# Kernel optimization log

Measured on AMD Instinct MI355X. Metric: run time of the kernel, lower is better.

Reference implementation:

```python
import jax, jax.numpy as jnp
import numpy as np

N_TYPES = 4
AEV_DIM = 384
HIDDEN = [160, 128, 96]
CELU_ALPHA = 0.1


def _init_params(key):
    dims = [AEV_DIM] + HIDDEN + [1]
    params = {}
    for li in range(len(dims) - 1):
        key, kw = jax.random.split(key)
        scale = 1.0 / np.sqrt(dims[li])
        # stacked over the N_TYPES per-atom-type experts
        params[f"W{li}"] = (jax.random.normal(kw, (N_TYPES, dims[li], dims[li + 1]), dtype=jnp.float32) * scale)
        params[f"b{li}"] = jnp.zeros((N_TYPES, dims[li + 1]), dtype=jnp.float32)
    return params


def setup_inputs() -> dict:
    key = jax.random.key(0)
    k1, k2, k3 = jax.random.split(key, 3)
    B, A = 2048, 64
    species = jax.random.randint(k1, (B, A), 0, N_TYPES, dtype=jnp.int64)
    aev = jax.random.normal(k2, (B, A, AEV_DIM), dtype=jnp.float32)
    inp = {"species": species, "aev": aev}
    inp.update(_init_params(k3))
    return inp


def _mlp(x, t, W0, b0, W1, b1, W2, b2, W3, b3):
    # x: [N, aev_dim] -> [N] per-atom energy for atom type t
    h = jax.nn.celu(x @ W0[t] + b0[t], alpha=CELU_ALPHA)
    h = jax.nn.celu(h @ W1[t] + b1[t], alpha=CELU_ALPHA)
    h = jax.nn.celu(h @ W2[t] + b2[t], alpha=CELU_ALPHA)
    return (h @ W3[t] + b3[t]).reshape(-1)


def reference(species, aev, W0, b0, W1, b1, W2, b2, W3, b3):
    B, A = species.shape
    sp = species.reshape(-1)            # [B*A]
    x = aev.reshape(-1, aev.shape[-1])  # [B*A, aev_dim]
    out = jnp.zeros(sp.shape, dtype=aev.dtype)  # padding_fill = 0
    for t in range(N_TYPES):  # fixed small expert set
        y = _mlp(x, t, W0, b0, W1, b1, W2, b2, W3, b3)
        out = jnp.where(sp == t, y, out)
    energies = out.reshape(B, A).sum(axis=1)  # reduce over atoms
    return species, energies
```

## Files before the change

### kernel.cpp

```cpp
#include <hip/hip_runtime.h>
#include <hip/hip_bf16.h>
#include <math.h>


#define NATOMS   131072
#define NMOL     2048
#define AEV      384
#define NTYPES   4
#define MBLK     64
#define PADTOT   (NATOMS + NTYPES * MBLK)
#define NBLK_MLP (PADTOT / MBLK)
#define NBLK_H   512

#define WB_L1 61440
#define WB_L2 81920
#define WB_T  94208

typedef __attribute__((ext_vector_type(8))) short bf16x8;
typedef __attribute__((ext_vector_type(4))) float f32x4;

__device__ __forceinline__ float celu01(float v) {
  return (v > 0.f) ? v : 0.1f * (__expf(v * 10.f) - 1.f);
}
__device__ __forceinline__ unsigned short f2bf(float x) {
  unsigned u = __float_as_uint(x);
  return (unsigned short)((u + 0x7FFFu + ((u >> 16) & 1u)) >> 16);
}
__device__ __forceinline__ unsigned int pk2(float lo, float hi) {
  union { __hip_bfloat162 h; unsigned int u; } c;
  c.h = __float22bfloat162_rn(make_float2(lo, hi));
  return c.u;
}
__device__ __forceinline__ bf16x8 cvt8(const float4 r0, const float4 r1) {
  union { unsigned int u[4]; bf16x8 v; } c;
  c.u[0] = pk2(r0.x, r0.y);
  c.u[1] = pk2(r0.z, r0.w);
  c.u[2] = pk2(r1.x, r1.y);
  c.u[3] = pk2(r1.z, r1.w);
  return c.v;
}
__device__ __forceinline__ void dma16(const unsigned short* g, unsigned short* l) {
  __builtin_amdgcn_global_load_lds(
      (const __attribute__((address_space(1))) void*)(g),
      (__attribute__((address_space(3))) void*)(l), 16, 0, 0);
}


__global__ void k_pre(const int* __restrict__ species, float* __restrict__ out,
                      int* __restrict__ perm, int* __restrict__ hist,
                      const float* __restrict__ W0, const float* __restrict__ W1,
                      const float* __restrict__ W2, unsigned short* __restrict__ WB) {
  const int tid = threadIdx.x, blk = blockIdx.x;
  const int i = blk * 256 + tid;
  perm[i] = -1;
  if (i < NATOMS) out[i] = (float)species[i];
  if (i < NMOL) out[NATOMS + i] = 0.f;

  for (int f = i; f < NTYPES * WB_T; f += PADTOT) {
    const int t = f / WB_T, e0 = f - t * WB_T;
    int base, NT, N;
    const float* W;
    if (e0 < WB_L1)      { base = 0;     NT = 10; N = 160; W = W0 + (size_t)t * AEV * 160; }
    else if (e0 < WB_L2) { base = WB_L1; NT = 8;  N = 128; W = W1 + (size_t)t * 160 * 128; }
    else                 { base = WB_L2; NT = 6;  N = 96;  W = W2 + (size_t)t * 128 * 96; }
    const int e = e0 - base, frag = e >> 9, r = e & 511, lane = r >> 3, j = r & 7;
    const int kt = frag / NT, nt = frag - kt * NT;
    const int k = kt * 32 + ((lane >> 4) << 3) + j, n = nt * 16 + (lane & 15);
    WB[(size_t)t * WB_T + e0] = f2bf(W[k * N + n]);
  }

  if (blk < NBLK_H) {
    const int sp = species[i];
    const int wv = tid >> 6;
    __shared__ int wc[4 * NTYPES];
#pragma unroll
    for (int t = 0; t < NTYPES; ++t) {
      const unsigned long long m = __ballot(sp == t);
      if ((tid & 63) == 0) wc[wv * NTYPES + t] = __popcll(m);
    }
    __syncthreads();
    if (tid < NTYPES)
      hist[tid * NBLK_H + blk] = wc[tid] + wc[4 + tid] + wc[8 + tid] + wc[12 + tid];
  }
}


__global__ void k_scan(const int* __restrict__ hist, int* __restrict__ poff,
                       int* __restrict__ boff) {
  __shared__ int tot[NTYPES], base[NTYPES];
  const int tid = threadIdx.x, wv = tid >> 6, lane = tid & 63;
  int s = 0;
  for (int c = 0; c < 8; ++c) s += hist[wv * NBLK_H + c * 64 + lane];
  for (int off = 32; off; off >>= 1) s += __shfl_down(s, off);
  if (lane == 0) tot[wv] = s;
  __syncthreads();
  if (tid == 0) {
    int acc = 0; poff[0] = 0;
    for (int t = 0; t < NTYPES; ++t) {
      base[t] = acc;
      acc += ((tot[t] + 63) >> 6) << 6;
      poff[t + 1] = acc;
    }
  }
  __syncthreads();
  int carry = base[wv];
  for (int c = 0; c < 8; ++c) {
    const int orig = hist[wv * NBLK_H + c * 64 + lane];
    int v = orig;
    for (int off = 1; off < 64; off <<= 1) {
      const int u = __shfl_up(v, off);
      if (lane >= off) v += u;
    }
    boff[wv * NBLK_H + c * 64 + lane] = carry + v - orig;
    carry += __shfl(v, 63);
  }
}

__global__ void k_scatter(const int* __restrict__ species, const int* __restrict__ boff,
                          int* __restrict__ perm) {
  const int tid = threadIdx.x, blk = blockIdx.x;
  const int i = blk * 256 + tid;
  const int sp = species[i];
  const int wv = tid >> 6;
  __shared__ int wc[4 * NTYPES];
  unsigned long long msel = 0;
#pragma unroll
  for (int t = 0; t < NTYPES; ++t) {
    const unsigned long long m = __ballot(sp == t);
    if ((tid & 63) == 0) wc[wv * NTYPES + t] = __popcll(m);
    if (sp == t) msel = m;
  }
  __syncthreads();
  int woff = 0;
  for (int w = 0; w < wv; ++w) woff += wc[w * NTYPES + sp];
  const int rk = __builtin_amdgcn_mbcnt_hi((unsigned)(msel >> 32),
                 __builtin_amdgcn_mbcnt_lo((unsigned)msel, 0));
  perm[boff[sp * NBLK_H + blk] + woff + rk] = i;
}


__global__ __launch_bounds__(128) void k_mlp(
    const float* __restrict__ aev, const unsigned short* __restrict__ WB,
    const float* __restrict__ b0, const float* __restrict__ b1,
    const float* __restrict__ b2, const float* __restrict__ b3,
    const float* __restrict__ W3,
    const int* __restrict__ poff, const int* __restrict__ perm,
    float* __restrict__ outE)
{
  __shared__ __align__(16) unsigned short H[64 * 168];
  __shared__ __align__(16) unsigned short WL[2][5120];
  __shared__ int permS[64];

  const int tid  = threadIdx.x;
  const int lane = tid & 63;
  const int wv   = __builtin_amdgcn_readfirstlane(tid >> 6);
  const int quad = lane >> 4, l15 = lane & 15;
  const int slot0 = blockIdx.x * MBLK;

  if (tid < 64) permS[tid] = perm[slot0 + tid];
  int t_ = (slot0 >= poff[1]) + (slot0 >= poff[2]) + (slot0 >= poff[3]);
  if (t_ > 3) t_ = 3;
  const int t = __builtin_amdgcn_readfirstlane(t_);

  const unsigned short* WBt = WB + (size_t)t * WB_T;

#pragma unroll
  for (int s = 0; s < 5; ++s)
    dma16(WBt + (wv * 5 + s) * 512 + lane * 8, &WL[0][(wv * 5 + s) * 512]);

  __syncthreads();

  const float* rp[2];
#pragma unroll
  for (int mtl = 0; mtl < 2; ++mtl) {
    const int ai = permS[(2 * wv + mtl) * 16 + l15];
    rp[mtl] = aev + (size_t)(ai < 0 ? 0 : ai) * AEV + quad * 8;
  }

  f32x4 acc0[10][2];
#pragma unroll
  for (int nt = 0; nt < 10; ++nt) {
    const float b = b0[t * 160 + nt * 16 + l15];
#pragma unroll
    for (int mtl = 0; mtl < 2; ++mtl) acc0[nt][mtl] = (f32x4){b, b, b, b};
  }

  float4 raw[2][2];
#pragma unroll
  for (int mtl = 0; mtl < 2; ++mtl) {
    raw[mtl][0] = *(const float4*)(rp[mtl]);
    raw[mtl][1] = *(const float4*)(rp[mtl] + 4);
  }

  for (int ks = 0; ks < 12; ++ks) {
    const int cur = ks & 1;
    const bf16x8 a0 = cvt8(raw[0][0], raw[0][1]);
    const bf16x8 a1 = cvt8(raw[1][0], raw[1][1]);
    if (ks < 11) {
#pragma unroll
      for (int mtl = 0; mtl < 2; ++mtl) {
        const float* p = rp[mtl] + (ks + 1) * 32;
        raw[mtl][0] = *(const float4*)p;
        raw[mtl][1] = *(const float4*)(p + 4);
      }
#pragma unroll
      for (int s = 0; s < 5; ++s)
        dma16(WBt + ((ks + 1) * 10 + wv * 5 + s) * 512 + lane * 8,
              &WL[cur ^ 1][(wv * 5 + s) * 512]);
    } else {
#pragma unroll
      for (int s = 0; s < 4; ++s)
        dma16(WBt + WB_L1 + (wv * 4 + s) * 512 + lane * 8,
              &WL[cur ^ 1][(wv * 4 + s) * 512]);
    }
#pragma unroll
    for (int nt = 0; nt < 10; ++nt) {
      const bf16x8 w = *(const bf16x8*)&WL[cur][nt * 512 + lane * 8];
      acc0[nt][0] = __builtin_amdgcn_mfma_f32_16x16x32_bf16(a0, w, acc0[nt][0], 0, 0, 0);
      acc0[nt][1] = __builtin_amdgcn_mfma_f32_16x16x32_bf16(a1, w, acc0[nt][1], 0, 0, 0);
    }
    __syncthreads();
  }

#pragma unroll
  for (int nt = 0; nt < 10; ++nt)
#pragma unroll
    for (int mtl = 0; mtl < 2; ++mtl)
#pragma unroll
      for (int r = 0; r < 4; ++r)
        H[((2 * wv + mtl) * 16 + quad * 4 + r) * 168 + nt * 16 + l15] = f2bf(celu01(acc0[nt][mtl][r]));
  __syncthreads();

  f32x4 acc1[8][2];
#pragma unroll
  for (int nt = 0; nt < 8; ++nt) {
    const float b = b1[t * 128 + nt * 16 + l15];
#pragma unroll
    for (int mtl = 0; mtl < 2; ++mtl) acc1[nt][mtl] = (f32x4){b, b, b, b};
  }
  for (int ks = 0; ks < 5; ++ks) {
    const int cur = ks & 1;
    const bf16x8 a0 = *(const bf16x8*)&H[((2 * wv + 0) * 16 + l15) * 168 + quad * 8 + ks * 32];
    const bf16x8 a1 = *(const bf16x8*)&H[((2 * wv + 1) * 16 + l15) * 168 + quad * 8 + ks * 32];
    if (ks < 4) {
#pragma unroll
      for (int s = 0; s < 4; ++s)
        dma16(WBt + WB_L1 + ((ks + 1) * 8 + wv * 4 + s) * 512 + lane * 8,
              &WL[cur ^ 1][(wv * 4 + s) * 512]);
    } else {
#pragma unroll
      for (int s = 0; s < 3; ++s)
        dma16(WBt + WB_L2 + (wv * 3 + s) * 512 + lane * 8,
              &WL[cur ^ 1][(wv * 3 + s) * 512]);
    }
#pragma unroll
    for (int nt = 0; nt < 8; ++nt) {
      const bf16x8 w = *(const bf16x8*)&WL[cur][nt * 512 + lane * 8];
      acc1[nt][0] = __builtin_amdgcn_mfma_f32_16x16x32_bf16(a0, w, acc1[nt][0], 0, 0, 0);
      acc1[nt][1] = __builtin_amdgcn_mfma_f32_16x16x32_bf16(a1, w, acc1[nt][1], 0, 0, 0);
    }
    __syncthreads();
  }
#pragma unroll
  for (int nt = 0; nt < 8; ++nt)
#pragma unroll
    for (int mtl = 0; mtl < 2; ++mtl)
#pragma unroll
      for (int r = 0; r < 4; ++r)
        H[((2 * wv + mtl) * 16 + quad * 4 + r) * 136 + nt * 16 + l15] = f2bf(celu01(acc1[nt][mtl][r]));
  __syncthreads();

  f32x4 acc2[6][2];
#pragma unroll
  for (int nt = 0; nt < 6; ++nt) {
    const float b = b2[t * 96 + nt * 16 + l15];
#pragma unroll
    for (int mtl = 0; mtl < 2; ++mtl) acc2[nt][mtl] = (f32x4){b, b, b, b};
  }
  for (int ks = 0; ks < 4; ++ks) {
    const int cur = (ks + 1) & 1;
    const bf16x8 a0 = *(const bf16x8*)&H[((2 * wv + 0) * 16 + l15) * 136 + quad * 8 + ks * 32];
    const bf16x8 a1 = *(const bf16x8*)&H[((2 * wv + 1) * 16 + l15) * 136 + quad * 8 + ks * 32];
    if (ks < 3) {
#pragma unroll
      for (int s = 0; s < 3; ++s)
        dma16(WBt + WB_L2 + ((ks + 1) * 6 + wv * 3 + s) * 512 + lane * 8,
              &WL[cur ^ 1][(wv * 3 + s) * 512]);
    }
#pragma unroll
    for (int nt = 0; nt < 6; ++nt) {
      const bf16x8 w = *(const bf16x8*)&WL[cur][nt * 512 + lane * 8];
      acc2[nt][0] = __builtin_amdgcn_mfma_f32_16x16x32_bf16(a0, w, acc2[nt][0], 0, 0, 0);
      acc2[nt][1] = __builtin_amdgcn_mfma_f32_16x16x32_bf16(a1, w, acc2[nt][1], 0, 0, 0);
    }
    __syncthreads();
  }
#pragma unroll
  for (int nt = 0; nt < 6; ++nt)
#pragma unroll
    for (int mtl = 0; mtl < 2; ++mtl)
#pragma unroll
      for (int r = 0; r < 4; ++r)
        H[((2 * wv + mtl) * 16 + quad * 4 + r) * 104 + nt * 16 + l15] = f2bf(celu01(acc2[nt][mtl][r]));
  __syncthreads();

  bf16x8 w3f[3];
#pragma unroll
  for (int ks = 0; ks < 3; ++ks) {
    const float* wp = W3 + t * 96 + ks * 32 + quad * 8;
    const float4 f0 = *(const float4*)wp;
    const float4 f1 = *(const float4*)(wp + 4);
    w3f[ks] = cvt8(f0, f1);
  }
  f32x4 accE[2];
#pragma unroll
  for (int mtl = 0; mtl < 2; ++mtl) accE[mtl] = (f32x4){0.f, 0.f, 0.f, 0.f};
#pragma unroll
  for (int mtl = 0; mtl < 2; ++mtl)
#pragma unroll
    for (int ks = 0; ks < 3; ++ks) {
      const bf16x8 a = *(const bf16x8*)&H[((2 * wv + mtl) * 16 + l15) * 104 + quad * 8 + ks * 32];
      accE[mtl] = __builtin_amdgcn_mfma_f32_16x16x32_bf16(a, w3f[ks], accE[mtl], 0, 0, 0);
    }
  const float bb3 = b3[t];
#pragma unroll
  for (int mtl = 0; mtl < 2; ++mtl)
#pragma unroll
    for (int r = 0; r < 4; ++r)
      if (l15 == 0) {
        const int ai = permS[(2 * wv + mtl) * 16 + quad * 4 + r];
        if (ai >= 0) atomicAdd(&outE[ai >> 6], accE[mtl][r] + bb3);
      }
}


extern "C" void kernel_launch(void* const* d_in, const int* in_sizes, int n_in,
                              void* d_out, int out_size, void* d_ws, size_t ws_size,
                              hipStream_t stream)
{
  const int*   species = (const int*)d_in[0];
  const float* aev     = (const float*)d_in[1];
  const float* W0 = (const float*)d_in[2];
  const float* b0 = (const float*)d_in[3];
  const float* W1 = (const float*)d_in[4];
  const float* b1 = (const float*)d_in[5];
  const float* W2 = (const float*)d_in[6];
  const float* b2 = (const float*)d_in[7];
  const float* W3 = (const float*)d_in[8];
  const float* b3 = (const float*)d_in[9];
  float* out = (float*)d_out;

  int* poff = (int*)d_ws;
  int* hist = poff + 8;
  int* boff = hist + NTYPES * NBLK_H;
  int* perm = boff + NTYPES * NBLK_H;
  unsigned short* WB = (unsigned short*)(perm + PADTOT);

  k_pre    <<<PADTOT / 256, 256, 0, stream>>>(species, out, perm, hist, W0, W1, W2, WB);
  k_scan   <<<1, 256, 0, stream>>>(hist, poff, boff);
  k_scatter<<<NBLK_H, 256, 0, stream>>>(species, boff, perm);
  k_mlp    <<<NBLK_MLP, 128, 0, stream>>>(aev, WB, b0, b1, b2, b3, W3,
                                          poff, perm, out + NATOMS);
}
```

Measured before the change: 367.3 us.

## Use single-wave MLP blocks loading weights directly from global memory

Shrinks each MLP block to one wavefront handling 32 atoms and drops the LDS double-buffered weight staging along with all block barriers. Weight fragments are now read straight from global memory, expected to hit in L2/L1, and the permutation indices move from LDS to wave shuffles. The goal is to remove synchronization overhead and LDS traffic and to raise occupancy through more, smaller blocks. In exchange, every wave re-fetches the full weight set per 32 rows, so global and cache traffic for weights roughly doubles, and MFMA issue may stall on load latency.

```diff
diff --git a/kernel.cpp b/kernel.cpp
--- a/kernel.cpp
+++ b/kernel.cpp
@@ -8,8 +8,9 @@
 #define AEV      384
 #define NTYPES   4
 #define MBLK     64
+#define MROWS    32
 #define PADTOT   (NATOMS + NTYPES * MBLK)
-#define NBLK_MLP (PADTOT / MBLK)
+#define NBLK_MLP (PADTOT / MROWS)
 #define NBLK_H   512
 
 #define WB_L1 61440
@@ -38,11 +39,6 @@
   c.u[2] = pk2(r1.x, r1.y);
   c.u[3] = pk2(r1.z, r1.w);
   return c.v;
-}
-__device__ __forceinline__ void dma16(const unsigned short* g, unsigned short* l) {
-  __builtin_amdgcn_global_load_lds(
-      (const __attribute__((address_space(1))) void*)(g),
-      (__attribute__((address_space(3))) void*)(l), 16, 0, 0);
 }
 
 
@@ -139,7 +135,7 @@
 }
 
 
-__global__ __launch_bounds__(128) void k_mlp(
+__global__ __launch_bounds__(64) void k_mlp(
     const float* __restrict__ aev, const unsigned short* __restrict__ WB,
     const float* __restrict__ b0, const float* __restrict__ b1,
     const float* __restrict__ b2, const float* __restrict__ b3,
@@ -147,35 +143,27 @@
     const int* __restrict__ poff, const int* __restrict__ perm,
     float* __restrict__ outE)
 {
-  __shared__ __align__(16) unsigned short H[64 * 168];
-  __shared__ __align__(16) unsigned short WL[2][5120];
-  __shared__ int permS[64];
-
-  const int tid  = threadIdx.x;
-  const int lane = tid & 63;
-  const int wv   = __builtin_amdgcn_readfirstlane(tid >> 6);
+  __shared__ __align__(16) unsigned short H[MROWS * 168];
+
+  const int lane = threadIdx.x;
   const int quad = lane >> 4, l15 = lane & 15;
-  const int slot0 = blockIdx.x * MBLK;
-
-  if (tid < 64) permS[tid] = perm[slot0 + tid];
+  const int slot0 = blockIdx.x * MROWS;
+
+  const int permv = perm[slot0 + (lane & 31)];
   int t_ = (slot0 >= poff[1]) + (slot0 >= poff[2]) + (slot0 >= poff[3]);
   if (t_ > 3) t_ = 3;
   const int t = __builtin_amdgcn_readfirstlane(t_);
 
-  const unsigned short* WBt = WB + (size_t)t * WB_T;
-
-#pragma unroll
-  for (int s = 0; s < 5; ++s)
-    dma16(WBt + (wv * 5 + s) * 512 + lane * 8, &WL[0][(wv * 5 + s) * 512]);
-
-  __syncthreads();
-
   const float* rp[2];
 #pragma unroll
   for (int mtl = 0; mtl < 2; ++mtl) {
-    const int ai = permS[(2 * wv + mtl) * 16 + l15];
+    const int ai = __shfl(permv, mtl * 16 + l15);
     rp[mtl] = aev + (size_t)(ai < 0 ? 0 : ai) * AEV + quad * 8;
   }
+
+  const bf16x8* wb0 = (const bf16x8*)(WB + (size_t)t * WB_T);
+  const bf16x8* wb1 = (const bf16x8*)(WB + (size_t)t * WB_T + WB_L1);
+  const bf16x8* wb2 = (const bf16x8*)(WB + (size_t)t * WB_T + WB_L2);
 
   f32x4 acc0[10][2];
 #pragma unroll
@@ -193,7 +181,6 @@
   }
 
   for (int ks = 0; ks < 12; ++ks) {
-    const int cur = ks & 1;
     const bf16x8 a0 = cvt8(raw[0][0], raw[0][1]);
     const bf16x8 a1 = cvt8(raw[1][0], raw[1][1]);
     if (ks < 11) {
@@ -203,33 +190,22 @@
         raw[mtl][0] = *(const float4*)p;
         raw[mtl][1] = *(const float4*)(p + 4);
       }
-#pragma unroll
-      for (int s = 0; s < 5; ++s)
-        dma16(WBt + ((ks + 1) * 10 + wv * 5 + s) * 512 + lane * 8,
-              &WL[cur ^ 1][(wv * 5 + s) * 512]);
-    } else {
-#pragma unroll
-      for (int s = 0; s < 4; ++s)
-        dma16(WBt + WB_L1 + (wv * 4 + s) * 512 + lane * 8,
-              &WL[cur ^ 1][(wv * 4 + s) * 512]);
     }
 #pragma unroll
     for (int nt = 0; nt < 10; ++nt) {
-      const bf16x8 w = *(const bf16x8*)&WL[cur][nt * 512 + lane * 8];
+      const bf16x8 w = wb0[(ks * 10 + nt) * 64 + lane];
       acc0[nt][0] = __builtin_amdgcn_mfma_f32_16x16x32_bf16(a0, w, acc0[nt][0], 0, 0, 0);
       acc0[nt][1] = __builtin_amdgcn_mfma_f32_16x16x32_bf16(a1, w, acc0[nt][1], 0, 0, 0);
     }
-    __syncthreads();
-  }
-
+  }
 #pragma unroll
   for (int nt = 0; nt < 10; ++nt)
 #pragma unroll
     for (int mtl = 0; mtl < 2; ++mtl)
 #pragma unroll
       for (int r = 0; r < 4; ++r)
-        H[((2 * wv + mtl) * 16 + quad * 4 + r) * 168 + nt * 16 + l15] = f2bf(celu01(acc0[nt][mtl][r]));
-  __syncthreads();
+        H[(mtl * 16 + quad * 4 + r) * 168 + nt * 16 + l15] = f2bf(celu01(acc0[nt][mtl][r]));
+  __builtin_amdgcn_sched_barrier(0);
 
   f32x4 acc1[8][2];
 #pragma unroll
@@ -238,37 +214,26 @@
 #pragma unroll
     for (int mtl = 0; mtl < 2; ++mtl) acc1[nt][mtl] = (f32x4){b, b, b, b};
   }
+#pragma unroll
   for (int ks = 0; ks < 5; ++ks) {
-    const int cur = ks & 1;
-    const bf16x8 a0 = *(const bf16x8*)&H[((2 * wv + 0) * 16 + l15) * 168 + quad * 8 + ks * 32];
-    const bf16x8 a1 = *(const bf16x8*)&H[((2 * wv + 1) * 16 + l15) * 168 + quad * 8 + ks * 32];
-    if (ks < 4) {
-#pragma unroll
-      for (int s = 0; s < 4; ++s)
-        dma16(WBt + WB_L1 + ((ks + 1) * 8 + wv * 4 + s) * 512 + lane * 8,
-              &WL[cur ^ 1][(wv * 4 + s) * 512]);
-    } else {
-#pragma unroll
-      for (int s = 0; s < 3; ++s)
-        dma16(WBt + WB_L2 + (wv * 3 + s) * 512 + lane * 8,
-              &WL[cur ^ 1][(wv * 3 + s) * 512]);
-    }
+    const bf16x8 a0 = *(const bf16x8*)&H[(0 * 16 + l15) * 168 + quad * 8 + ks * 32];
+    const bf16x8 a1 = *(const bf16x8*)&H[(1 * 16 + l15) * 168 + quad * 8 + ks * 32];
 #pragma unroll
     for (int nt = 0; nt < 8; ++nt) {
-      const bf16x8 w = *(const bf16x8*)&WL[cur][nt * 512 + lane * 8];
+      const bf16x8 w = wb1[(ks * 8 + nt) * 64 + lane];
       acc1[nt][0] = __builtin_amdgcn_mfma_f32_16x16x32_bf16(a0, w, acc1[nt][0], 0, 0, 0);
       acc1[nt][1] = __builtin_amdgcn_mfma_f32_16x16x32_bf16(a1, w, acc1[nt][1], 0, 0, 0);
     }
-    __syncthreads();
-  }
+  }
+  __builtin_amdgcn_sched_barrier(0);
 #pragma unroll
   for (int nt = 0; nt < 8; ++nt)
 #pragma unroll
     for (int mtl = 0; mtl < 2; ++mtl)
 #pragma unroll
       for (int r = 0; r < 4; ++r)
-        H[((2 * wv + mtl) * 16 + quad * 4 + r) * 136 + nt * 16 + l15] = f2bf(celu01(acc1[nt][mtl][r]));
-  __syncthreads();
+        H[(mtl * 16 + quad * 4 + r) * 136 + nt * 16 + l15] = f2bf(celu01(acc1[nt][mtl][r]));
+  __builtin_amdgcn_sched_barrier(0);
 
   f32x4 acc2[6][2];
 #pragma unroll
@@ -277,32 +242,26 @@
 #pragma unroll
     for (int mtl = 0; mtl < 2; ++mtl) acc2[nt][mtl] = (f32x4){b, b, b, b};
   }
+#pragma unroll
   for (int ks = 0; ks < 4; ++ks) {
-    const int cur = (ks + 1) & 1;
-    const bf16x8 a0 = *(const bf16x8*)&H[((2 * wv + 0) * 16 + l15) * 136 + quad * 8 + ks * 32];
-    const bf16x8 a1 = *(const bf16x8*)&H[((2 * wv + 1) * 16 + l15) * 136 + quad * 8 + ks * 32];
-    if (ks < 3) {
-#pragma unroll
-      for (int s = 0; s < 3; ++s)
-        dma16(WBt + WB_L2 + ((ks + 1) * 6 + wv * 3 + s) * 512 + lane * 8,
-              &WL[cur ^ 1][(wv * 3 + s) * 512]);
-    }
+    const bf16x8 a0 = *(const bf16x8*)&H[(0 * 16 + l15) * 136 + quad * 8 + ks * 32];
+    const bf16x8 a1 = *(const bf16x8*)&H[(1 * 16 + l15) * 136 + quad * 8 + ks * 32];
 #pragma unroll
     for (int nt = 0; nt < 6; ++nt) {
-      const bf16x8 w = *(const bf16x8*)&WL[cur][nt * 512 + lane * 8];
+      const bf16x8 w = wb2[(ks * 6 + nt) * 64 + lane];
       acc2[nt][0] = __builtin_amdgcn_mfma_f32_16x16x32_bf16(a0, w, acc2[nt][0], 0, 0, 0);
       acc2[nt][1] = __builtin_amdgcn_mfma_f32_16x16x32_bf16(a1, w, acc2[nt][1], 0, 0, 0);
     }
-    __syncthreads();
-  }
+  }
+  __builtin_amdgcn_sched_barrier(0);
 #pragma unroll
   for (int nt = 0; nt < 6; ++nt)
 #pragma unroll
     for (int mtl = 0; mtl < 2; ++mtl)
 #pragma unroll
       for (int r = 0; r < 4; ++r)
-        H[((2 * wv + mtl) * 16 + quad * 4 + r) * 104 + nt * 16 + l15] = f2bf(celu01(acc2[nt][mtl][r]));
-  __syncthreads();
+        H[(mtl * 16 + quad * 4 + r) * 104 + nt * 16 + l15] = f2bf(celu01(acc2[nt][mtl][r]));
+  __builtin_amdgcn_sched_barrier(0);
 
   bf16x8 w3f[3];
 #pragma unroll
@@ -319,18 +278,17 @@
   for (int mtl = 0; mtl < 2; ++mtl)
 #pragma unroll
     for (int ks = 0; ks < 3; ++ks) {
-      const bf16x8 a = *(const bf16x8*)&H[((2 * wv + mtl) * 16 + l15) * 104 + quad * 8 + ks * 32];
+      const bf16x8 a = *(const bf16x8*)&H[(mtl * 16 + l15) * 104 + quad * 8 + ks * 32];
       accE[mtl] = __builtin_amdgcn_mfma_f32_16x16x32_bf16(a, w3f[ks], accE[mtl], 0, 0, 0);
     }
   const float bb3 = b3[t];
 #pragma unroll
   for (int mtl = 0; mtl < 2; ++mtl)
 #pragma unroll
-    for (int r = 0; r < 4; ++r)
-      if (l15 == 0) {
-        const int ai = permS[(2 * wv + mtl) * 16 + quad * 4 + r];
-        if (ai >= 0) atomicAdd(&outE[ai >> 6], accE[mtl][r] + bb3);
-      }
+    for (int r = 0; r < 4; ++r) {
+      const int ai = __shfl(permv, mtl * 16 + quad * 4 + r);
+      if (l15 == 0 && ai >= 0) atomicAdd(&outE[ai >> 6], accE[mtl][r] + bb3);
+    }
 }
 
 
@@ -359,6 +317,6 @@
   k_pre    <<<PADTOT / 256, 256, 0, stream>>>(species, out, perm, hist, W0, W1, W2, WB);
   k_scan   <<<1, 256, 0, stream>>>(hist, poff, boff);
   k_scatter<<<NBLK_H, 256, 0, stream>>>(species, boff, perm);
-  k_mlp    <<<NBLK_MLP, 128, 0, stream>>>(aev, WB, b0, b1, b2, b3, W3,
-                                          poff, perm, out + NATOMS);
-}
+  k_mlp    <<<NBLK_MLP, 64, 0, stream>>>(aev, WB, b0, b1, b2, b3, W3,
+                                         poff, perm, out + NATOMS);
+}
```

New measurement: 430.2 us. 1.17x slower.
